# Kernel tuning notes

Measured on AMD Instinct MI355X. Metric: run time of the kernel, lower is better.

## Reference

```python
import jax, jax.numpy as jnp
import numpy as np

BS = 32  # leaf block size
NUM_HOPS = 1  # ATTENTION_HOPS


def setup_inputs() -> dict:
    key = jax.random.key(0)
    ks = jax.random.split(key, 10)
    B, N, C, H = 1, 131072, 256, 4
    E = 8 * N
    x = jax.random.normal(ks[0], (B, N, C), dtype=jnp.float32)
    rows = jax.random.randint(ks[1], (E,), 0, N)
    offs = jax.random.randint(ks[2], (E,), 0, BS)
    cols = (rows // BS) * BS + offs  # in-block neighbors
    edge_index = jnp.stack([rows, cols]).astype(jnp.int64)
    edge_values = jax.random.normal(ks[3], (E,), dtype=jnp.float32)
    positions = jax.random.uniform(ks[4], (N, 3), dtype=jnp.float32)
    qkv_w = jax.random.normal(ks[5], (3 * C, C), dtype=jnp.float32) * 0.02
    qkv_b = jnp.zeros((3 * C,), dtype=jnp.float32)
    proj_w = jax.random.normal(ks[6], (C, C), dtype=jnp.float32) * 0.02
    proj_b = jnp.zeros((C,), dtype=jnp.float32)
    gate_w = jax.random.normal(ks[7], (H, 4), dtype=jnp.float32) * 0.01  # init std=0.01
    gate_b = jnp.zeros((H,), dtype=jnp.float32)
    return {"x": x, "edge_index": edge_index, "edge_values": edge_values,
            "positions": positions, "qkv_w": qkv_w, "qkv_b": qkv_b,
            "proj_w": proj_w, "proj_b": proj_b, "gate_w": gate_w, "gate_b": gate_b}


def _connectivity(edge_index, edge_values, positions, nb):
    rows, cols = edge_index[0], edge_index[1]
    br, bc = rows // BS, cols // BS
    in_block = (br == bc) & (br < nb)
    r_l, c_l = rows % BS, cols % BS
    b_safe = jnp.where(in_block, br, nb)  # out-of-range -> dropped by scatter
    dx = positions[cols] - positions[rows]            # [E,3]
    ef_flat = jnp.concatenate([dx, edge_values[:, None]], axis=1)  # [E,4]
    adj = jnp.zeros((nb, BS, BS), jnp.float32).at[b_safe, r_l, c_l].set(1.0, mode='drop')
    eye = jnp.eye(BS, dtype=jnp.float32)
    reachable = jnp.broadcast_to(eye[None], (nb, BS, BS))
    cur = adj
    for _ in range(NUM_HOPS):
        reachable = jnp.clip(reachable + cur, 0.0, 1.0)
        cur = jnp.matmul(cur, adj)
    attn_mask = jnp.concatenate([reachable, jnp.ones((nb, BS, 1), jnp.float32)], axis=2)
    edge_feats = jnp.zeros((nb, BS, BS + 1, 4), jnp.float32)
    edge_feats = edge_feats.at[b_safe, r_l, c_l, :].set(ef_flat, mode='drop')
    return attn_mask, edge_feats


def reference(x, edge_index, edge_values, positions, qkv_w, qkv_b, proj_w, proj_b, gate_w, gate_b):
    B, N, C = x.shape
    H = gate_w.shape[0]
    hd = C // H
    scale = hd ** -0.5
    nb = N // BS  # N chosen divisible by BS (no pad)
    attn_mask, edge_feats = _connectivity(edge_index, edge_values, positions, nb)

    x_blk = x.reshape(B, nb, BS, C)
    block_node = x_blk.mean(axis=2, keepdims=True)
    kv = jnp.concatenate([x_blk, block_node], axis=2)  # [B,nb,BS+1,C]
    qkv_q = x_blk @ qkv_w.T + qkv_b
    qkv_kv = kv @ qkv_w.T + qkv_b
    q = qkv_q[..., :C].reshape(B, nb, BS, H, hd)
    k = qkv_kv[..., C:2 * C].reshape(B, nb, BS + 1, H, hd)
    v = qkv_kv[..., 2 * C:].reshape(B, nb, BS + 1, H, hd)

    scores = jnp.einsum('bnqhd,bnkhd->bnqkh', q, k) * scale

    ar = jnp.arange(BS)
    bias_physics = edge_feats.at[:, :, BS, :].set(0.0).at[:, :, BS, 3].set(1.0)
    bias_physics = bias_physics.at[:, ar, ar, :].set(0.0).at[:, ar, ar, 3].set(1.0)

    scores = scores + bias_physics[None, ..., 3:4]
    mask = attn_mask[None, :, :, :, None]  # [1,nb,BS,BS+1,1]
    scores = jnp.where(mask == 0, -jnp.inf, scores)
    attn_probs = jax.nn.softmax(scores, axis=3)

    gate = bias_physics @ gate_w.T + gate_b  # [nb,BS,BS+1,H]
    gate = jnp.where(mask == 0, 0.0, gate[None])
    combined = attn_probs + gate

    x_out = jnp.einsum('bnqkh,bnkhd->bnqhd', combined, v).reshape(B, nb, BS, C)
    out = x_out.reshape(B, N, C) @ proj_w.T + proj_b
    return out
```

## Files before the change

kernel.cpp:

```cpp
#include <hip/hip_runtime.h>
#include <math.h>

#define BSZ 32
#define CH  256

typedef short  bf16x8 __attribute__((ext_vector_type(8)));
typedef float  f32x4  __attribute__((ext_vector_type(4)));
typedef unsigned short ushort_t;
typedef unsigned int   uint_t;

#define MFMA(a, b, c) __builtin_amdgcn_mfma_f32_16x16x32_bf16((a), (b), (c), 0, 0, 0)

__device__ __forceinline__ ushort_t f2b(float f) {
    uint_t u = __builtin_bit_cast(uint_t, f);
    uint_t r = (u + 0x7FFFu + ((u >> 16) & 1u)) >> 16;
    return (ushort_t)r;
}
__device__ __forceinline__ float b2f(ushort_t u) {
    uint_t v = ((uint_t)u) << 16;
    return __builtin_bit_cast(float, v);
}
__device__ __forceinline__ uint_t pk2(float a, float b) {
    return (uint_t)f2b(a) | ((uint_t)f2b(b) << 16);
}

__global__ void edge_win_kernel(const int* __restrict__ ei, int E, int nb,
                                int* __restrict__ win) {
    int e = blockIdx.x * blockDim.x + threadIdx.x;
    if (e >= E) return;
    int r = ei[e];
    int c = ei[E + e];
    int br = r >> 5, bc = c >> 5;
    if (br == bc && br < nb) {
        atomicMax(&win[br * (BSZ * BSZ) + (r & 31) * BSZ + (c & 31)], e);
    }
}

__global__ void edge_feat_kernel(const int* __restrict__ ei,
                                 const float* __restrict__ ev,
                                 const float* __restrict__ pos,
                                 const int* __restrict__ win, int E,
                                 ushort_t* __restrict__ cellinfo) {
    int e = blockIdx.x * blockDim.x + threadIdx.x;
    if (e >= E) return;
    int r = ei[e];
    int c = ei[E + e];
    int br = r >> 5, bc = c >> 5;
    if (br != bc) return;
    int cell = br * 1024 + (r & 31) * 32 + (c & 31);
    if (win[cell] != e) return;
    float d0 = pos[c * 3 + 0] - pos[r * 3 + 0];
    float d1 = pos[c * 3 + 1] - pos[r * 3 + 1];
    float d2 = pos[c * 3 + 2] - pos[r * 3 + 2];
    float d3 = ev[e];
    uint2 w; w.x = pk2(d0, d1); w.y = pk2(d2, d3);
    *(uint2*)&cellinfo[(size_t)cell * 4] = w;
}

__global__ void wconv_kernel(const float* __restrict__ qkv_w,
                             const float* __restrict__ proj_w,
                             ushort_t* __restrict__ qkv_wf,
                             ushort_t* __restrict__ proj_wf) {
    int i = blockIdx.x * blockDim.x + threadIdx.x;
    int lane = i & 63, ks = (i >> 6) & 7, tile = i >> 9;
    int l15 = lane & 15, lg = lane >> 4;
    if (tile < 48) {
        const float* src = qkv_w + (size_t)(tile * 16 + l15) * 256 + ks * 32 + lg * 8;
        ushort_t* dst = qkv_wf + (size_t)i * 8;
        #pragma unroll
        for (int e = 0; e < 8; ++e) dst[e] = f2b(src[e]);
    }
    if (tile < 16) {
        const float* src = proj_w + (size_t)(tile * 16 + l15) * 256 + ks * 32 + lg * 8;
        ushort_t* dst = proj_wf + (size_t)i * 8;
        #pragma unroll
        for (int e = 0; e < 8; ++e) dst[e] = f2b(src[e]);
    }
}

#define LS_XB   0
#define LS_XO   16384
#define LS_CELL 32768
#define LS_SCR  40960
#define LS_TOT  45824

__global__ __launch_bounds__(256, 3)
void fused_attn(const float* __restrict__ x,
                const ushort_t* __restrict__ qkv_wf,
                const float* __restrict__ qkv_b,
                const ushort_t* __restrict__ cellinfo,
                const ushort_t* __restrict__ proj_wf,
                const float* __restrict__ proj_b,
                const float* __restrict__ gate_w,
                const float* __restrict__ gate_b,
                float* __restrict__ out)
{
    __shared__ __align__(16) char smem[LS_TOT];
    ushort_t* xb    = (ushort_t*)(smem + LS_XB);
    ushort_t* xo    = (ushort_t*)(smem + LS_XO);
    ushort_t* cellL = (ushort_t*)(smem + LS_CELL);

    const int t = threadIdx.x;
    const int h = t >> 6, lane = t & 63, l15 = lane & 15, lg = lane >> 4;
    const int bi = blockIdx.x, mbase = bi * 32;
    ushort_t* scr = (ushort_t*)(smem + LS_SCR + h * 1216);

    #pragma unroll
    for (int i = 0; i < 8; ++i) {
        int flat = i * 1024 + t * 4;
        int r = flat >> 8, c = flat & 255;
        float4 xv = *(const float4*)&x[(size_t)(mbase + r) * CH + c];
        uint2 wv; wv.x = pk2(xv.x, xv.y); wv.y = pk2(xv.z, xv.w);
        *(uint2*)&xb[r * 256 + (c ^ ((r & 7) << 3))] = wv;
    }
    #pragma unroll
    for (int i = 0; i < 2; ++i) {
        int pid = t * 2 + i;
        int qi = pid >> 4, p = pid & 15;
        uint4 cv = *(const uint4*)&cellinfo[(size_t)bi * 4096 + qi * 128 + p * 8];
        *(uint4*)&cellL[qi * 128 + ((p ^ (qi & 15)) * 8)] = cv;
    }
    __syncthreads();

    const int slB = (l15 & 7) << 3;
    const f32x4 zf = {0.f, 0.f, 0.f, 0.f};
    f32x4 acc[4][2];
    bf16x8 xfA[2], xfB[2], wfA[4], wfB[4];

#define LOADX2(dst, kss) { int k0_ = (((kss) * 32) + lg * 8) ^ slB;           \
        dst[0] = *(const bf16x8*)&xb[l15 * 256 + k0_];                        \
        dst[1] = *(const bf16x8*)&xb[(16 + l15) * 256 + k0_]; }

#define LOADW4(dst, tb, kss) { _Pragma("unroll")                              \
        for (int ti_ = 0; ti_ < 4; ++ti_)                                     \
            dst[ti_] = *(const bf16x8*)(qkv_wf                                \
                + ((size_t)(((tb) + ti_) * 8 + (kss))) * 512 + lane * 8); }

#define COMP4(xf, wf, SW) { _Pragma("unroll")                                 \
        for (int ti_ = 0; ti_ < 4; ++ti_) {                                   \
            if (SW) {                                                         \
                acc[ti_][0] = MFMA(wf[ti_], xf[0], acc[ti_][0]);              \
                acc[ti_][1] = MFMA(wf[ti_], xf[1], acc[ti_][1]);              \
            } else {                                                          \
                acc[ti_][0] = MFMA(xf[0], wf[ti_], acc[ti_][0]);              \
                acc[ti_][1] = MFMA(xf[1], wf[ti_], acc[ti_][1]);              \
            } } }

#define GEMM_PHASE(TB, SW) {                                                  \
    _Pragma("unroll")                                                         \
    for (int a_ = 0; a_ < 4; ++a_) { acc[a_][0] = zf; acc[a_][1] = zf; }      \
    LOADX2(xfA, 0); LOADW4(wfA, TB, 0);                                       \
    LOADX2(xfB, 1); LOADW4(wfB, TB, 1);                                       \
    COMP4(xfA, wfA, SW);                                                      \
    LOADX2(xfA, 2); LOADW4(wfA, TB, 2);                                       \
    COMP4(xfB, wfB, SW);                                                      \
    LOADX2(xfB, 3); LOADW4(wfB, TB, 3);                                       \
    COMP4(xfA, wfA, SW);                                                      \
    LOADX2(xfA, 4); LOADW4(wfA, TB, 4);                                       \
    COMP4(xfB, wfB, SW);                                                      \
    LOADX2(xfB, 5); LOADW4(wfB, TB, 5);                                       \
    COMP4(xfA, wfA, SW);                                                      \
    LOADX2(xfA, 6); LOADW4(wfA, TB, 6);                                       \
    COMP4(xfB, wfB, SW);                                                      \
    LOADX2(xfB, 7); LOADW4(wfB, TB, 7);                                       \
    COMP4(xfA, wfA, SW);                                                      \
    COMP4(xfB, wfB, SW); }

    auto repack16 = [&](f32x4 a0, f32x4 a1) -> bf16x8 {
        uint2 w0, w1;
        w0.x = pk2(a0[0], a0[1]); w0.y = pk2(a0[2], a0[3]);
        w1.x = pk2(a1[0], a1[1]); w1.y = pk2(a1[2], a1[3]);
        *(uint2*)&scr[l15 * 38 + lg * 4]      = w0;
        *(uint2*)&scr[l15 * 38 + 16 + lg * 4] = w1;
        return *(const bf16x8*)&scr[l15 * 38 + lg * 8];
    };

    bf16x8 qld[2][2], kld[2][2], vf[4], cfr[2];
    GEMM_PHASE(h * 4, true);
    #pragma unroll
    for (int ti = 0; ti < 4; ++ti) {
        f32x4 bq = *(const f32x4*)&qkv_b[(h * 4 + ti) * 16 + lg * 4];
        acc[ti][0] += bq; acc[ti][1] += bq;
    }
    #pragma unroll
    for (int qt = 0; qt < 2; ++qt)
        #pragma unroll
        for (int ks2 = 0; ks2 < 2; ++ks2)
            qld[qt][ks2] = repack16(acc[ks2 * 2][qt], acc[ks2 * 2 + 1][qt]);

    GEMM_PHASE(16 + h * 4, true);
    #pragma unroll
    for (int ti = 0; ti < 4; ++ti) {
        f32x4 bk = *(const f32x4*)&qkv_b[256 + (h * 4 + ti) * 16 + lg * 4];
        acc[ti][0] += bk; acc[ti][1] += bk;
    }
    #pragma unroll
    for (int kt = 0; kt < 2; ++kt)
        #pragma unroll
        for (int ks2 = 0; ks2 < 2; ++ks2)
            kld[kt][ks2] = repack16(acc[ks2 * 2][kt], acc[ks2 * 2 + 1][kt]);

    GEMM_PHASE(32 + h * 4, false);
    #pragma unroll
    for (int ct = 0; ct < 4; ++ct) {
        float bvs = qkv_b[512 + (h * 4 + ct) * 16 + l15];
        f32x4 bb = {bvs, bvs, bvs, bvs};
        acc[ct][0] += bb; acc[ct][1] += bb;
        vf[ct] = repack16(acc[ct][0], acc[ct][1]);
    }

    f32x4 s[2][2];
    #pragma unroll
    for (int qt = 0; qt < 2; ++qt) { s[qt][0] = zf; s[qt][1] = zf; }
    #pragma unroll
    for (int qt = 0; qt < 2; ++qt)
        #pragma unroll
        for (int ks2 = 0; ks2 < 2; ++ks2)
            #pragma unroll
            for (int kt = 0; kt < 2; ++kt)
                s[qt][kt] = MFMA(kld[kt][ks2], qld[qt][ks2], s[qt][kt]);

    const float gw0 = gate_w[h * 4 + 0], gw1 = gate_w[h * 4 + 1];
    const float gw2 = gate_w[h * 4 + 2], gw3 = gate_w[h * 4 + 3];
    const float gb  = gate_b[h];
    #pragma unroll
    for (int qt = 0; qt < 2; ++qt) {
        int qi = qt * 16 + l15;
        float r[8], gt[8];
        float rawsum = 0.f;
        #pragma unroll
        for (int kt = 0; kt < 2; ++kt) {
            int kj0 = kt * 16 + lg * 4;
            int pb2 = kt * 8 + lg * 2;
            uint4 cA = *(const uint4*)&cellL[qi * 128 + ((pb2 ^ (qi & 15)) * 8)];
            uint4 cB = *(const uint4*)&cellL[qi * 128 + (((pb2 + 1) ^ (qi & 15)) * 8)];
            uint_t d01[4] = {cA.x, cA.z, cB.x, cB.z};
            uint_t d23[4] = {cA.y, cA.w, cB.y, cB.w};
            #pragma unroll
            for (int j = 0; j < 4; ++j) {
                int kj = kj0 + j;
                bool fixed = (kj == qi);
                ushort_t e3b = (ushort_t)(d23[j] >> 16);
                bool valid = (e3b != (ushort_t)0xFFFFu);
                float e3 = b2f(e3b);
                float sb = fixed ? 1.0f : (valid ? e3 : -INFINITY);
                float g;
                if (fixed)      g = gw3 + gb;
                else if (valid) g = b2f((ushort_t)(d01[j] & 0xFFFF)) * gw0
                                  + b2f((ushort_t)(d01[j] >> 16))    * gw1
                                  + b2f((ushort_t)(d23[j] & 0xFFFF)) * gw2
                                  + e3 * gw3 + gb;
                else            g = 0.0f;
                float sraw = s[qt][kt][j];
                rawsum += sraw;
                r[kt * 4 + j]  = sraw * 0.125f + sb;
                gt[kt * 4 + j] = g;
            }
        }
        rawsum += __shfl_xor(rawsum, 16);
        rawsum += __shfl_xor(rawsum, 32);
        float r2 = rawsum * (0.125f / 32.0f) + 1.0f;

        float m = fmaxf(fmaxf(fmaxf(r[0], r[1]), fmaxf(r[2], r[3])),
                        fmaxf(fmaxf(r[4], r[5]), fmaxf(r[6], r[7])));
        m = fmaxf(m, r2);
        m = fmaxf(m, __shfl_xor(m, 16));
        m = fmaxf(m, __shfl_xor(m, 32));
        float sum = 0.f;
        #pragma unroll
        for (int i = 0; i < 8; ++i) { r[i] = __expf(r[i] - m); sum += r[i]; }
        sum += __shfl_xor(sum, 16);
        sum += __shfl_xor(sum, 32);
        float e2 = __expf(r2 - m);
        float inv = 1.0f / (sum + e2);
        float comb32 = e2 * inv + (gw3 + gb);
        float cadd = comb32 * 0.03125f;
        f32x4 ra = {r[0] * inv + gt[0] + cadd, r[1] * inv + gt[1] + cadd,
                    r[2] * inv + gt[2] + cadd, r[3] * inv + gt[3] + cadd};
        f32x4 rb = {r[4] * inv + gt[4] + cadd, r[5] * inv + gt[5] + cadd,
                    r[6] * inv + gt[6] + cadd, r[7] * inv + gt[7] + cadd};
        cfr[qt] = repack16(ra, rb);
    }

    #pragma unroll
    for (int ct = 0; ct < 4; ++ct) {
        #pragma unroll
        for (int qt = 0; qt < 2; ++qt) {
            f32x4 a2 = zf;
            a2 = MFMA(vf[ct], cfr[qt], a2);
            int qi = qt * 16 + l15;
            uint2 wv;
            wv.x = pk2(a2[0], a2[1]);
            wv.y = pk2(a2[2], a2[3]);
            int c0 = h * 64 + ct * 16 + lg * 4;
            *(uint2*)&xo[qi * 256 + (c0 ^ ((l15 & 7) << 3))] = wv;
        }
    }
    __syncthreads();

    {
        const int slR = (l15 & 7) << 3;
        bf16x8 pwA[4], pwB[4];
        f32x4 pacc[4][2];
        #pragma unroll
        for (int i = 0; i < 4; ++i) { pacc[i][0] = zf; pacc[i][1] = zf; }

#define LOADPW(dst, kss) { _Pragma("unroll")                                  \
        for (int i_ = 0; i_ < 4; ++i_)                                        \
            dst[i_] = *(const bf16x8*)(proj_wf                                \
                + ((size_t)((h * 4 + i_) * 8 + (kss))) * 512 + lane * 8); }

#define PCOMP(pw, kss) { int k0_ = (kss) * 32 + lg * 8;                       \
        bf16x8 b0_ = *(const bf16x8*)&xo[l15 * 256 + (k0_ ^ slR)];            \
        bf16x8 b1_ = *(const bf16x8*)&xo[(16 + l15) * 256 + (k0_ ^ slR)];     \
        _Pragma("unroll")                                                     \
        for (int i_ = 0; i_ < 4; ++i_) {                                      \
            pacc[i_][0] = MFMA(pw[i_], b0_, pacc[i_][0]);                     \
            pacc[i_][1] = MFMA(pw[i_], b1_, pacc[i_][1]);                     \
        } }

        LOADPW(pwA, 0); LOADPW(pwB, 1);
        PCOMP(pwA, 0);  LOADPW(pwA, 2);
        PCOMP(pwB, 1);  LOADPW(pwB, 3);
        PCOMP(pwA, 2);  LOADPW(pwA, 4);
        PCOMP(pwB, 3);  LOADPW(pwB, 5);
        PCOMP(pwA, 4);  LOADPW(pwA, 6);
        PCOMP(pwB, 5);  LOADPW(pwB, 7);
        PCOMP(pwA, 6);
        PCOMP(pwB, 7);

        #pragma unroll
        for (int i = 0; i < 4; ++i) {
            int n0 = (h * 4 + i) * 16;
            f32x4 bv = *(const f32x4*)&proj_b[n0 + lg * 4];
            f32x4 o0 = pacc[i][0] + bv;
            f32x4 o1 = pacc[i][1] + bv;
            *(f32x4*)&out[(size_t)(mbase + l15) * 256 + n0 + lg * 4]      = o0;
            *(f32x4*)&out[(size_t)(mbase + 16 + l15) * 256 + n0 + lg * 4] = o1;
        }
    }
}

extern "C" void kernel_launch(void* const* d_in, const int* in_sizes, int n_in,
                              void* d_out, int out_size, void* d_ws, size_t ws_size,
                              hipStream_t stream) {
    const float* x      = (const float*)d_in[0];
    const int*   ei     = (const int*)  d_in[1];
    const float* ev     = (const float*)d_in[2];
    const float* pos    = (const float*)d_in[3];
    const float* qkv_w  = (const float*)d_in[4];
    const float* qkv_b  = (const float*)d_in[5];
    const float* proj_w = (const float*)d_in[6];
    const float* proj_b = (const float*)d_in[7];
    const float* gate_w = (const float*)d_in[8];
    const float* gate_b = (const float*)d_in[9];
    float* out = (float*)d_out;

    const int E  = in_sizes[2];
    const int N  = in_sizes[0] / CH;
    const int nb = N / BSZ;

    char* ws = (char*)d_ws;
    int*      win      = (int*)ws;
    ushort_t* cellinfo = (ushort_t*)(ws + (size_t)nb * 4096);
    size_t off = (size_t)nb * 12288;
    ushort_t* qkv_wf  = (ushort_t*)(ws + off); off += 48 * 8 * 64 * 8 * 2;
    ushort_t* proj_wf = (ushort_t*)(ws + off); off += 16 * 8 * 64 * 8 * 2;

    hipMemsetAsync(ws, 0xFF, (size_t)nb * 12288, stream);
    edge_win_kernel<<<(E + 255) / 256, 256, 0, stream>>>(ei, E, nb, win);
    edge_feat_kernel<<<(E + 255) / 256, 256, 0, stream>>>(ei, ev, pos, win, E,
                                                          cellinfo);
    wconv_kernel<<<96, 256, 0, stream>>>(qkv_w, proj_w, qkv_wf, proj_wf);
    fused_attn<<<nb, 256, 0, stream>>>(x, qkv_wf, qkv_b, cellinfo,
                                       proj_wf, proj_b, gate_w, gate_b, out);
}
```

Measured before the change: 276.6 us.

## Drop edge-feature pass via per-node gate projection and process two blocks per workgroup

The per-edge feature kernel and its packed cell buffer are removed. The gate's position term is now computed as a per-node projection (pg) and evaluated as pg[col]-pg[row]; edge values are gathered directly from the winning edge index inside the fused kernel. The fused kernel now handles 64 rows (two leaf blocks) per workgroup, which reuses each weight load across twice as many rows. It also shares LDS between xb and xo and adds s_setprio around the MFMA sections. In exchange there are more registers per thread (launch bounds drop to 2 waves per SIMD) and a scattered gather of edge values in the attention phase.

```diff
diff --git a/kernel.cpp b/kernel.cpp
--- a/kernel.cpp
+++ b/kernel.cpp
@@ -36,25 +36,15 @@
     }
 }
 
-__global__ void edge_feat_kernel(const int* __restrict__ ei,
-                                 const float* __restrict__ ev,
-                                 const float* __restrict__ pos,
-                                 const int* __restrict__ win, int E,
-                                 ushort_t* __restrict__ cellinfo) {
-    int e = blockIdx.x * blockDim.x + threadIdx.x;
-    if (e >= E) return;
-    int r = ei[e];
-    int c = ei[E + e];
-    int br = r >> 5, bc = c >> 5;
-    if (br != bc) return;
-    int cell = br * 1024 + (r & 31) * 32 + (c & 31);
-    if (win[cell] != e) return;
-    float d0 = pos[c * 3 + 0] - pos[r * 3 + 0];
-    float d1 = pos[c * 3 + 1] - pos[r * 3 + 1];
-    float d2 = pos[c * 3 + 2] - pos[r * 3 + 2];
-    float d3 = ev[e];
-    uint2 w; w.x = pk2(d0, d1); w.y = pk2(d2, d3);
-    *(uint2*)&cellinfo[(size_t)cell * 4] = w;
+__global__ void pgate_kernel(const float* __restrict__ pos,
+                             const float* __restrict__ gate_w,
+                             float* __restrict__ pg, int N) {
+    int n = blockIdx.x * 256 + threadIdx.x;
+    int h = blockIdx.y;
+    if (n >= N) return;
+    pg[(size_t)h * N + n] = pos[n * 3 + 0] * gate_w[h * 4 + 0]
+                          + pos[n * 3 + 1] * gate_w[h * 4 + 1]
+                          + pos[n * 3 + 2] * gate_w[h * 4 + 2];
 }
 
 __global__ void wconv_kernel(const float* __restrict__ qkv_w,
@@ -78,93 +68,43 @@
     }
 }
 
-#define LS_XB   0
-#define LS_XO   16384
-#define LS_CELL 32768
-#define LS_SCR  40960
-#define LS_TOT  45824
-
-__global__ __launch_bounds__(256, 3)
+#define LS_SCR 32768
+#define LS_TOT 37632
+
+__global__ __launch_bounds__(256, 2)
 void fused_attn(const float* __restrict__ x,
                 const ushort_t* __restrict__ qkv_wf,
                 const float* __restrict__ qkv_b,
-                const ushort_t* __restrict__ cellinfo,
+                const int* __restrict__ win,
+                const float* __restrict__ ev,
+                const float* __restrict__ pg,
                 const ushort_t* __restrict__ proj_wf,
                 const float* __restrict__ proj_b,
                 const float* __restrict__ gate_w,
                 const float* __restrict__ gate_b,
-                float* __restrict__ out)
+                float* __restrict__ out, int N)
 {
     __shared__ __align__(16) char smem[LS_TOT];
-    ushort_t* xb    = (ushort_t*)(smem + LS_XB);
-    ushort_t* xo    = (ushort_t*)(smem + LS_XO);
-    ushort_t* cellL = (ushort_t*)(smem + LS_CELL);
+    ushort_t* xb = (ushort_t*)(smem);
+    ushort_t* xo = (ushort_t*)(smem);
 
     const int t = threadIdx.x;
     const int h = t >> 6, lane = t & 63, l15 = lane & 15, lg = lane >> 4;
-    const int bi = blockIdx.x, mbase = bi * 32;
+    const int bi = blockIdx.x, mbase = bi * 64;
     ushort_t* scr = (ushort_t*)(smem + LS_SCR + h * 1216);
 
     #pragma unroll
-    for (int i = 0; i < 8; ++i) {
+    for (int i = 0; i < 16; ++i) {
         int flat = i * 1024 + t * 4;
         int r = flat >> 8, c = flat & 255;
         float4 xv = *(const float4*)&x[(size_t)(mbase + r) * CH + c];
         uint2 wv; wv.x = pk2(xv.x, xv.y); wv.y = pk2(xv.z, xv.w);
         *(uint2*)&xb[r * 256 + (c ^ ((r & 7) << 3))] = wv;
     }
-    #pragma unroll
-    for (int i = 0; i < 2; ++i) {
-        int pid = t * 2 + i;
-        int qi = pid >> 4, p = pid & 15;
-        uint4 cv = *(const uint4*)&cellinfo[(size_t)bi * 4096 + qi * 128 + p * 8];
-        *(uint4*)&cellL[qi * 128 + ((p ^ (qi & 15)) * 8)] = cv;
-    }
     __syncthreads();
 
     const int slB = (l15 & 7) << 3;
     const f32x4 zf = {0.f, 0.f, 0.f, 0.f};
-    f32x4 acc[4][2];
-    bf16x8 xfA[2], xfB[2], wfA[4], wfB[4];
-
-#define LOADX2(dst, kss) { int k0_ = (((kss) * 32) + lg * 8) ^ slB;           \
-        dst[0] = *(const bf16x8*)&xb[l15 * 256 + k0_];                        \
-        dst[1] = *(const bf16x8*)&xb[(16 + l15) * 256 + k0_]; }
-
-#define LOADW4(dst, tb, kss) { _Pragma("unroll")                              \
-        for (int ti_ = 0; ti_ < 4; ++ti_)                                     \
-            dst[ti_] = *(const bf16x8*)(qkv_wf                                \
-                + ((size_t)(((tb) + ti_) * 8 + (kss))) * 512 + lane * 8); }
-
-#define COMP4(xf, wf, SW) { _Pragma("unroll")                                 \
-        for (int ti_ = 0; ti_ < 4; ++ti_) {                                   \
-            if (SW) {                                                         \
-                acc[ti_][0] = MFMA(wf[ti_], xf[0], acc[ti_][0]);              \
-                acc[ti_][1] = MFMA(wf[ti_], xf[1], acc[ti_][1]);              \
-            } else {                                                          \
-                acc[ti_][0] = MFMA(xf[0], wf[ti_], acc[ti_][0]);              \
-                acc[ti_][1] = MFMA(xf[1], wf[ti_], acc[ti_][1]);              \
-            } } }
-
-#define GEMM_PHASE(TB, SW) {                                                  \
-    _Pragma("unroll")                                                         \
-    for (int a_ = 0; a_ < 4; ++a_) { acc[a_][0] = zf; acc[a_][1] = zf; }      \
-    LOADX2(xfA, 0); LOADW4(wfA, TB, 0);                                       \
-    LOADX2(xfB, 1); LOADW4(wfB, TB, 1);                                       \
-    COMP4(xfA, wfA, SW);                                                      \
-    LOADX2(xfA, 2); LOADW4(wfA, TB, 2);                                       \
-    COMP4(xfB, wfB, SW);                                                      \
-    LOADX2(xfB, 3); LOADW4(wfB, TB, 3);                                       \
-    COMP4(xfA, wfA, SW);                                                      \
-    LOADX2(xfA, 4); LOADW4(wfA, TB, 4);                                       \
-    COMP4(xfB, wfB, SW);                                                      \
-    LOADX2(xfB, 5); LOADW4(wfB, TB, 5);                                       \
-    COMP4(xfA, wfA, SW);                                                      \
-    LOADX2(xfA, 6); LOADW4(wfA, TB, 6);                                       \
-    COMP4(xfB, wfB, SW);                                                      \
-    LOADX2(xfB, 7); LOADW4(wfB, TB, 7);                                       \
-    COMP4(xfA, wfA, SW);                                                      \
-    COMP4(xfB, wfB, SW); }
 
     auto repack16 = [&](f32x4 a0, f32x4 a1) -> bf16x8 {
         uint2 w0, w1;
@@ -175,135 +115,207 @@
         return *(const bf16x8*)&scr[l15 * 38 + lg * 8];
     };
 
-    bf16x8 qld[2][2], kld[2][2], vf[4], cfr[2];
-    GEMM_PHASE(h * 4, true);
+    bf16x8 qld[2][2][2], kld[2][2][2], vf[2][4];
+
+#define QK_SECTION(TB, DST)                                                   \
+    _Pragma("unroll")                                                         \
+    for (int p = 0; p < 2; ++p) {                                             \
+        const int T0 = (TB) + p * 2, T1 = T0 + 1;                             \
+        bf16x8 W0[8], W1[8];                                                  \
+        _Pragma("unroll")                                                     \
+        for (int ks = 0; ks < 8; ++ks) {                                      \
+            W0[ks] = *(const bf16x8*)(qkv_wf                                  \
+                        + ((size_t)(T0 * 8 + ks)) * 512 + lane * 8);          \
+            W1[ks] = *(const bf16x8*)(qkv_wf                                  \
+                        + ((size_t)(T1 * 8 + ks)) * 512 + lane * 8);          \
+        }                                                                     \
+        f32x4 a0[4], a1[4];                                                   \
+        _Pragma("unroll")                                                     \
+        for (int m = 0; m < 4; ++m) { a0[m] = zf; a1[m] = zf; }               \
+        __builtin_amdgcn_s_setprio(1);                                        \
+        _Pragma("unroll")                                                     \
+        for (int ks = 0; ks < 8; ++ks) {                                      \
+            int k0 = (ks * 32 + lg * 8) ^ slB;                                \
+            _Pragma("unroll")                                                 \
+            for (int m = 0; m < 4; ++m) {                                     \
+                bf16x8 xf = *(const bf16x8*)&xb[(m * 16 + l15) * 256 + k0];   \
+                a0[m] = MFMA(W0[ks], xf, a0[m]);                              \
+                a1[m] = MFMA(W1[ks], xf, a1[m]);                              \
+            }                                                                 \
+        }                                                                     \
+        __builtin_amdgcn_s_setprio(0);                                        \
+        f32x4 b0v = *(const f32x4*)&qkv_b[T0 * 16 + lg * 4];                  \
+        f32x4 b1v = *(const f32x4*)&qkv_b[T1 * 16 + lg * 4];                  \
+        _Pragma("unroll")                                                     \
+        for (int m = 0; m < 4; ++m) { a0[m] += b0v; a1[m] += b1v; }           \
+        _Pragma("unroll")                                                     \
+        for (int gl = 0; gl < 2; ++gl)                                        \
+            _Pragma("unroll")                                                 \
+            for (int rt = 0; rt < 2; ++rt)                                    \
+                DST[gl][rt][p] = repack16(a0[gl * 2 + rt], a1[gl * 2 + rt]);  \
+    }
+
+    QK_SECTION(h * 4, qld)
+    QK_SECTION(16 + h * 4, kld)
+
+    uint4  wv4[2][2][2];
+    float4 pgc[2][2];
+    float  pgr[2][2];
     #pragma unroll
-    for (int ti = 0; ti < 4; ++ti) {
-        f32x4 bq = *(const f32x4*)&qkv_b[(h * 4 + ti) * 16 + lg * 4];
-        acc[ti][0] += bq; acc[ti][1] += bq;
-    }
-    #pragma unroll
-    for (int qt = 0; qt < 2; ++qt)
-        #pragma unroll
-        for (int ks2 = 0; ks2 < 2; ++ks2)
-            qld[qt][ks2] = repack16(acc[ks2 * 2][qt], acc[ks2 * 2 + 1][qt]);
-
-    GEMM_PHASE(16 + h * 4, true);
-    #pragma unroll
-    for (int ti = 0; ti < 4; ++ti) {
-        f32x4 bk = *(const f32x4*)&qkv_b[256 + (h * 4 + ti) * 16 + lg * 4];
-        acc[ti][0] += bk; acc[ti][1] += bk;
-    }
-    #pragma unroll
-    for (int kt = 0; kt < 2; ++kt)
-        #pragma unroll
-        for (int ks2 = 0; ks2 < 2; ++ks2)
-            kld[kt][ks2] = repack16(acc[ks2 * 2][kt], acc[ks2 * 2 + 1][kt]);
-
-    GEMM_PHASE(32 + h * 4, false);
+    for (int gl = 0; gl < 2; ++gl) {
+        int cb = mbase + gl * 32;
+        #pragma unroll
+        for (int qt = 0; qt < 2; ++qt) {
+            int qi = qt * 16 + l15;
+            wv4[gl][qt][0] = *(const uint4*)&win[(size_t)(bi * 2 + gl) * 1024
+                                                + qi * 32 + lg * 4];
+            wv4[gl][qt][1] = *(const uint4*)&win[(size_t)(bi * 2 + gl) * 1024
+                                                + qi * 32 + 16 + lg * 4];
+            pgr[gl][qt] = pg[(size_t)h * N + cb + qi];
+        }
+        pgc[gl][0] = *(const float4*)&pg[(size_t)h * N + cb + lg * 4];
+        pgc[gl][1] = *(const float4*)&pg[(size_t)h * N + cb + 16 + lg * 4];
+    }
+
     #pragma unroll
     for (int ct = 0; ct < 4; ++ct) {
-        float bvs = qkv_b[512 + (h * 4 + ct) * 16 + l15];
+        int T = 32 + h * 4 + ct;
+        bf16x8 W[8];
+        #pragma unroll
+        for (int ks = 0; ks < 8; ++ks)
+            W[ks] = *(const bf16x8*)(qkv_wf + ((size_t)(T * 8 + ks)) * 512 + lane * 8);
+        f32x4 a[4];
+        #pragma unroll
+        for (int m = 0; m < 4; ++m) a[m] = zf;
+        __builtin_amdgcn_s_setprio(1);
+        #pragma unroll
+        for (int ks = 0; ks < 8; ++ks) {
+            int k0 = (ks * 32 + lg * 8) ^ slB;
+            #pragma unroll
+            for (int m = 0; m < 4; ++m) {
+                bf16x8 xf = *(const bf16x8*)&xb[(m * 16 + l15) * 256 + k0];
+                a[m] = MFMA(xf, W[ks], a[m]);
+            }
+        }
+        __builtin_amdgcn_s_setprio(0);
+        float bvs = qkv_b[T * 16 + l15];
         f32x4 bb = {bvs, bvs, bvs, bvs};
-        acc[ct][0] += bb; acc[ct][1] += bb;
-        vf[ct] = repack16(acc[ct][0], acc[ct][1]);
-    }
-
-    f32x4 s[2][2];
+        #pragma unroll
+        for (int m = 0; m < 4; ++m) a[m] += bb;
+        vf[0][ct] = repack16(a[0], a[1]);
+        vf[1][ct] = repack16(a[2], a[3]);
+    }
+    __syncthreads();
+
+    const float gw3v = gate_w[h * 4 + 3];
+    const float gbv  = gate_b[h];
+    const float g3b  = gw3v + gbv;
+
     #pragma unroll
-    for (int qt = 0; qt < 2; ++qt) { s[qt][0] = zf; s[qt][1] = zf; }
-    #pragma unroll
-    for (int qt = 0; qt < 2; ++qt)
-        #pragma unroll
-        for (int ks2 = 0; ks2 < 2; ++ks2)
-            #pragma unroll
-            for (int kt = 0; kt < 2; ++kt)
-                s[qt][kt] = MFMA(kld[kt][ks2], qld[qt][ks2], s[qt][kt]);
-
-    const float gw0 = gate_w[h * 4 + 0], gw1 = gate_w[h * 4 + 1];
-    const float gw2 = gate_w[h * 4 + 2], gw3 = gate_w[h * 4 + 3];
-    const float gb  = gate_b[h];
-    #pragma unroll
-    for (int qt = 0; qt < 2; ++qt) {
-        int qi = qt * 16 + l15;
-        float r[8], gt[8];
-        float rawsum = 0.f;
-        #pragma unroll
-        for (int kt = 0; kt < 2; ++kt) {
-            int kj0 = kt * 16 + lg * 4;
-            int pb2 = kt * 8 + lg * 2;
-            uint4 cA = *(const uint4*)&cellL[qi * 128 + ((pb2 ^ (qi & 15)) * 8)];
-            uint4 cB = *(const uint4*)&cellL[qi * 128 + (((pb2 + 1) ^ (qi & 15)) * 8)];
-            uint_t d01[4] = {cA.x, cA.z, cB.x, cB.z};
-            uint_t d23[4] = {cA.y, cA.w, cB.y, cB.w};
-            #pragma unroll
-            for (int j = 0; j < 4; ++j) {
-                int kj = kj0 + j;
-                bool fixed = (kj == qi);
-                ushort_t e3b = (ushort_t)(d23[j] >> 16);
-                bool valid = (e3b != (ushort_t)0xFFFFu);
-                float e3 = b2f(e3b);
-                float sb = fixed ? 1.0f : (valid ? e3 : -INFINITY);
-                float g;
-                if (fixed)      g = gw3 + gb;
-                else if (valid) g = b2f((ushort_t)(d01[j] & 0xFFFF)) * gw0
-                                  + b2f((ushort_t)(d01[j] >> 16))    * gw1
-                                  + b2f((ushort_t)(d23[j] & 0xFFFF)) * gw2
-                                  + e3 * gw3 + gb;
-                else            g = 0.0f;
-                float sraw = s[qt][kt][j];
-                rawsum += sraw;
-                r[kt * 4 + j]  = sraw * 0.125f + sb;
-                gt[kt * 4 + j] = g;
-            }
-        }
-        rawsum += __shfl_xor(rawsum, 16);
-        rawsum += __shfl_xor(rawsum, 32);
-        float r2 = rawsum * (0.125f / 32.0f) + 1.0f;
-
-        float m = fmaxf(fmaxf(fmaxf(r[0], r[1]), fmaxf(r[2], r[3])),
-                        fmaxf(fmaxf(r[4], r[5]), fmaxf(r[6], r[7])));
-        m = fmaxf(m, r2);
-        m = fmaxf(m, __shfl_xor(m, 16));
-        m = fmaxf(m, __shfl_xor(m, 32));
-        float sum = 0.f;
-        #pragma unroll
-        for (int i = 0; i < 8; ++i) { r[i] = __expf(r[i] - m); sum += r[i]; }
-        sum += __shfl_xor(sum, 16);
-        sum += __shfl_xor(sum, 32);
-        float e2 = __expf(r2 - m);
-        float inv = 1.0f / (sum + e2);
-        float comb32 = e2 * inv + (gw3 + gb);
-        float cadd = comb32 * 0.03125f;
-        f32x4 ra = {r[0] * inv + gt[0] + cadd, r[1] * inv + gt[1] + cadd,
-                    r[2] * inv + gt[2] + cadd, r[3] * inv + gt[3] + cadd};
-        f32x4 rb = {r[4] * inv + gt[4] + cadd, r[5] * inv + gt[5] + cadd,
-                    r[6] * inv + gt[6] + cadd, r[7] * inv + gt[7] + cadd};
-        cfr[qt] = repack16(ra, rb);
-    }
-
-    #pragma unroll
-    for (int ct = 0; ct < 4; ++ct) {
+    for (int gl = 0; gl < 2; ++gl) {
+        float evv[2][8];
+        #pragma unroll
+        for (int qt = 0; qt < 2; ++qt)
+            #pragma unroll
+            for (int kt = 0; kt < 2; ++kt) {
+                const int* wp = (const int*)&wv4[gl][qt][kt];
+                #pragma unroll
+                for (int j = 0; j < 4; ++j) {
+                    int e = wp[j];
+                    evv[qt][kt * 4 + j] = ev[e < 0 ? 0 : e];
+                }
+            }
+
+        f32x4 s[2][2];
+        #pragma unroll
+        for (int qt = 0; qt < 2; ++qt) { s[qt][0] = zf; s[qt][1] = zf; }
+        __builtin_amdgcn_s_setprio(1);
+        #pragma unroll
+        for (int qt = 0; qt < 2; ++qt)
+            #pragma unroll
+            for (int p = 0; p < 2; ++p)
+                #pragma unroll
+                for (int kt = 0; kt < 2; ++kt)
+                    s[qt][kt] = MFMA(kld[gl][kt][p], qld[gl][qt][p], s[qt][kt]);
+        __builtin_amdgcn_s_setprio(0);
+
+        bf16x8 cfr[2];
         #pragma unroll
         for (int qt = 0; qt < 2; ++qt) {
-            f32x4 a2 = zf;
-            a2 = MFMA(vf[ct], cfr[qt], a2);
             int qi = qt * 16 + l15;
-            uint2 wv;
-            wv.x = pk2(a2[0], a2[1]);
-            wv.y = pk2(a2[2], a2[3]);
-            int c0 = h * 64 + ct * 16 + lg * 4;
-            *(uint2*)&xo[qi * 256 + (c0 ^ ((l15 & 7) << 3))] = wv;
-        }
+            float r[8], gt[8];
+            float rawsum = 0.f;
+            #pragma unroll
+            for (int kt = 0; kt < 2; ++kt) {
+                const int* wp = (const int*)&wv4[gl][qt][kt];
+                #pragma unroll
+                for (int j = 0; j < 4; ++j) {
+                    int kj = kt * 16 + lg * 4 + j;
+                    bool fixed = (kj == qi);
+                    bool valid = wp[j] >= 0;
+                    float e3 = evv[qt][kt * 4 + j];
+                    float sb = fixed ? 1.0f : (valid ? e3 : -INFINITY);
+                    float pgcv = ((const float*)&pgc[gl][kt])[j];
+                    float g = fixed ? g3b
+                            : (valid ? (pgcv - pgr[gl][qt] + e3 * gw3v + gbv) : 0.0f);
+                    float sraw = s[qt][kt][j];
+                    rawsum += sraw;
+                    r[kt * 4 + j]  = sraw * 0.125f + sb;
+                    gt[kt * 4 + j] = g;
+                }
+            }
+            rawsum += __shfl_xor(rawsum, 16);
+            rawsum += __shfl_xor(rawsum, 32);
+            float r2 = rawsum * (0.125f / 32.0f) + 1.0f;
+
+            float m = fmaxf(fmaxf(fmaxf(r[0], r[1]), fmaxf(r[2], r[3])),
+                            fmaxf(fmaxf(r[4], r[5]), fmaxf(r[6], r[7])));
+            m = fmaxf(m, r2);
+            m = fmaxf(m, __shfl_xor(m, 16));
+            m = fmaxf(m, __shfl_xor(m, 32));
+            float sum = 0.f;
+            #pragma unroll
+            for (int i = 0; i < 8; ++i) { r[i] = __expf(r[i] - m); sum += r[i]; }
+            sum += __shfl_xor(sum, 16);
+            sum += __shfl_xor(sum, 32);
+            float e2 = __expf(r2 - m);
+            float inv = 1.0f / (sum + e2);
+            float comb32 = e2 * inv + g3b;
+            float cadd = comb32 * 0.03125f;
+            f32x4 ra = {r[0] * inv + gt[0] + cadd, r[1] * inv + gt[1] + cadd,
+                        r[2] * inv + gt[2] + cadd, r[3] * inv + gt[3] + cadd};
+            f32x4 rb = {r[4] * inv + gt[4] + cadd, r[5] * inv + gt[5] + cadd,
+                        r[6] * inv + gt[6] + cadd, r[7] * inv + gt[7] + cadd};
+            cfr[qt] = repack16(ra, rb);
+        }
+
+        __builtin_amdgcn_s_setprio(1);
+        #pragma unroll
+        for (int ct = 0; ct < 4; ++ct) {
+            #pragma unroll
+            for (int qt = 0; qt < 2; ++qt) {
+                f32x4 a2 = zf;
+                a2 = MFMA(vf[gl][ct], cfr[qt], a2);
+                int qi = qt * 16 + l15;
+                uint2 wv;
+                wv.x = pk2(a2[0], a2[1]);
+                wv.y = pk2(a2[2], a2[3]);
+                int c0 = h * 64 + ct * 16 + lg * 4;
+                *(uint2*)&xo[gl * 8192 + qi * 256 + (c0 ^ ((l15 & 7) << 3))] = wv;
+            }
+        }
+        __builtin_amdgcn_s_setprio(0);
     }
     __syncthreads();
 
     {
         const int slR = (l15 & 7) << 3;
         bf16x8 pwA[4], pwB[4];
-        f32x4 pacc[4][2];
-        #pragma unroll
-        for (int i = 0; i < 4; ++i) { pacc[i][0] = zf; pacc[i][1] = zf; }
+        f32x4 pacc[4][4];
+        #pragma unroll
+        for (int i = 0; i < 4; ++i)
+            #pragma unroll
+            for (int rt = 0; rt < 4; ++rt) pacc[i][rt] = zf;
 
 #define LOADPW(dst, kss) { _Pragma("unroll")                                  \
         for (int i_ = 0; i_ < 4; ++i_)                                        \
@@ -311,15 +323,17 @@
                 + ((size_t)((h * 4 + i_) * 8 + (kss))) * 512 + lane * 8); }
 
 #define PCOMP(pw, kss) { int k0_ = (kss) * 32 + lg * 8;                       \
-        bf16x8 b0_ = *(const bf16x8*)&xo[l15 * 256 + (k0_ ^ slR)];            \
-        bf16x8 b1_ = *(const bf16x8*)&xo[(16 + l15) * 256 + (k0_ ^ slR)];     \
-        _Pragma("unroll")                                                     \
-        for (int i_ = 0; i_ < 4; ++i_) {                                      \
-            pacc[i_][0] = MFMA(pw[i_], b0_, pacc[i_][0]);                     \
-            pacc[i_][1] = MFMA(pw[i_], b1_, pacc[i_][1]);                     \
+        _Pragma("unroll")                                                     \
+        for (int rt_ = 0; rt_ < 4; ++rt_) {                                   \
+            bf16x8 b_ = *(const bf16x8*)&xo[(rt_ >> 1) * 8192                 \
+                         + ((rt_ & 1) * 16 + l15) * 256 + (k0_ ^ slR)];       \
+            _Pragma("unroll")                                                 \
+            for (int i_ = 0; i_ < 4; ++i_)                                    \
+                pacc[i_][rt_] = MFMA(pw[i_], b_, pacc[i_][rt_]);              \
         } }
 
         LOADPW(pwA, 0); LOADPW(pwB, 1);
+        __builtin_amdgcn_s_setprio(1);
         PCOMP(pwA, 0);  LOADPW(pwA, 2);
         PCOMP(pwB, 1);  LOADPW(pwB, 3);
         PCOMP(pwA, 2);  LOADPW(pwA, 4);
@@ -328,15 +342,18 @@
         PCOMP(pwB, 5);  LOADPW(pwB, 7);
         PCOMP(pwA, 6);
         PCOMP(pwB, 7);
+        __builtin_amdgcn_s_setprio(0);
 
         #pragma unroll
         for (int i = 0; i < 4; ++i) {
             int n0 = (h * 4 + i) * 16;
             f32x4 bv = *(const f32x4*)&proj_b[n0 + lg * 4];
-            f32x4 o0 = pacc[i][0] + bv;
-            f32x4 o1 = pacc[i][1] + bv;
-            *(f32x4*)&out[(size_t)(mbase + l15) * 256 + n0 + lg * 4]      = o0;
-            *(f32x4*)&out[(size_t)(mbase + 16 + l15) * 256 + n0 + lg * 4] = o1;
+            #pragma unroll
+            for (int rt = 0; rt < 4; ++rt) {
+                f32x4 o = pacc[i][rt] + bv;
+                int row = mbase + (rt >> 1) * 32 + (rt & 1) * 16 + l15;
+                *(f32x4*)&out[(size_t)row * 256 + n0 + lg * 4] = o;
+            }
         }
     }
 }
@@ -361,17 +378,17 @@
     const int nb = N / BSZ;
 
     char* ws = (char*)d_ws;
-    int*      win      = (int*)ws;
-    ushort_t* cellinfo = (ushort_t*)(ws + (size_t)nb * 4096);
-    size_t off = (size_t)nb * 12288;
+    int*   win = (int*)ws;
+    float* pg  = (float*)(ws + (size_t)nb * 4096);
+    size_t off = (size_t)nb * 4096 + (size_t)4 * N * 4;
     ushort_t* qkv_wf  = (ushort_t*)(ws + off); off += 48 * 8 * 64 * 8 * 2;
     ushort_t* proj_wf = (ushort_t*)(ws + off); off += 16 * 8 * 64 * 8 * 2;
 
-    hipMemsetAsync(ws, 0xFF, (size_t)nb * 12288, stream);
+    hipMemsetAsync(win, 0xFF, (size_t)nb * 4096, stream);
     edge_win_kernel<<<(E + 255) / 256, 256, 0, stream>>>(ei, E, nb, win);
-    edge_feat_kernel<<<(E + 255) / 256, 256, 0, stream>>>(ei, ev, pos, win, E,
-                                                          cellinfo);
+    pgate_kernel<<<dim3((N + 255) / 256, 4), 256, 0, stream>>>(pos, gate_w, pg, N);
     wconv_kernel<<<96, 256, 0, stream>>>(qkv_w, proj_w, qkv_wf, proj_wf);
-    fused_attn<<<nb, 256, 0, stream>>>(x, qkv_wf, qkv_b, cellinfo,
-                                       proj_wf, proj_b, gate_w, gate_b, out);
-}
+    fused_attn<<<nb / 2, 256, 0, stream>>>(x, qkv_wf, qkv_b, win, ev, pg,
+                                           proj_wf, proj_b, gate_w, gate_b,
+                                           out, N);
+}
```

Measured after the change: 238.8 us. 1.16x faster.
